# Performance work log

Hardware: AMD Instinct MI355X
Metric: run time of the kernel (lower is better)

The kernel has to match this reference:

```python
import jax, jax.numpy as jnp
import numpy as np

EPS = 1e-5
B, C, N = 2, 256, 65536


def conv1x1(x, W, b):
    # Conv1d with kernel_size=1: (B,Cin,N) x (Cout,Cin) -> (B,Cout,N)
    return jnp.einsum('oc,bcn->bon', W, x) + b[None, :, None]


def instance_norm(x):
    # InstanceNorm1d, affine=False, biased variance over the spatial dim
    m = jnp.mean(x, axis=-1, keepdims=True)
    v = jnp.var(x, axis=-1, keepdims=True)
    return (x - m) * jax.lax.rsqrt(v + EPS)


def mesh_conv(x, gemm, W, b):
    # MeshCNN MeshConv: gather self + 4 one-ring neighbor edges, symmetric fns, (1,5) conv.
    Bb, Cc, E = x.shape
    xp = jnp.concatenate([jnp.zeros((Bb, Cc, 1), x.dtype), x], axis=2)  # pad slot 0 (for -1/missing)
    eid = jnp.broadcast_to(jnp.arange(E, dtype=gemm.dtype)[None, :, None], (Bb, E, 1))
    Gi = jnp.concatenate([eid, gemm], axis=2) + 1                      # (B,E,5), +1 shift for pad row
    xt = xp.transpose(0, 2, 1)                                          # (B,E+1,C)
    f = jax.vmap(lambda xb, gb: xb[gb])(xt, Gi)                         # (B,E,5,C) gather
    f = f.transpose(0, 3, 1, 2)                                         # (B,C,E,5)
    f0, f1, f2, f3, f4 = (f[..., i] for i in range(5))
    g = jnp.stack([f0, f1 + f3, f2 + f4, jnp.abs(f1 - f3), jnp.abs(f2 - f4)], axis=-1)
    # Conv2d(Cin,Cout,(1,5)) over (B,C,E,5) -> (B,Cout,E)
    return jnp.einsum('ock,bcek->boe', W, g) + b[None, :, None]


def setup_inputs() -> dict:
    key = jax.random.key(0)
    ks = jax.random.split(key, 20)
    s = 0.05
    inp = {
        'x_0': jax.random.normal(ks[0], (B, C, N), jnp.float32),
        'x_1': jax.random.normal(ks[1], (B, C, N), jnp.float32),
        'gemm': jax.random.randint(ks[2], (B, N, 4), 0, N, jnp.int32),
        # conv_a / conv_b: C -> C//4
        'Wa': jax.random.normal(ks[3], (C // 4, C), jnp.float32) * s,
        'ba': jax.random.normal(ks[4], (C // 4,), jnp.float32) * s,
        'Wb': jax.random.normal(ks[5], (C // 4, C), jnp.float32) * s,
        'bb': jax.random.normal(ks[6], (C // 4,), jnp.float32) * s,
        # conv_a_local / conv_b_local: C//2 -> C//2
        'Wal': jax.random.normal(ks[7], (C // 2, C // 2), jnp.float32) * s,
        'bal': jax.random.normal(ks[8], (C // 2,), jnp.float32) * s,
        'Wbl': jax.random.normal(ks[9], (C // 2, C // 2), jnp.float32) * s,
        'bbl': jax.random.normal(ks[10], (C // 2,), jnp.float32) * s,
        # MeshConv weights: (Cout, Cin, 5)
        'Wat': jax.random.normal(ks[11], (C // 2, C // 2, 5), jnp.float32) * s,
        'bat': jax.random.normal(ks[12], (C // 2,), jnp.float32) * s,
        'Wbt': jax.random.normal(ks[13], (C // 2, C // 2, 5), jnp.float32) * s,
        'bbt': jax.random.normal(ks[14], (C // 2,), jnp.float32) * s,
        # fuse convs: C -> C
        'Waf': jax.random.normal(ks[15], (C, C), jnp.float32) * s,
        'baf': jax.random.normal(ks[16], (C,), jnp.float32) * s,
        'Wbf': jax.random.normal(ks[17], (C, C), jnp.float32) * s,
        'bbf': jax.random.normal(ks[18], (C,), jnp.float32) * s,
    }
    return inp


def reference(x_0, x_1, gemm, Wa, ba, Wb, bb, Wal, bal, Wbl, bbl,
              Wat, bat, Wbt, bbt, Waf, baf, Wbf, bbf):
    x_a = conv1x1(x_0, Wa, ba)
    x_b = conv1x1(x_1, Wb, bb)
    x_all = jnp.concatenate([x_a, x_b], axis=1)          # (B, C/2, N)
    a_local = conv1x1(x_all, Wal, bal)
    a_tri = mesh_conv(x_all, gemm, Wat, bat)
    x_a_two = jnp.concatenate([a_local, a_tri], axis=1)  # (B, C, N)
    b_local = conv1x1(x_all, Wbl, bbl)
    b_tri = mesh_conv(x_all, gemm, Wbt, bbt)
    x_b_two = jnp.concatenate([b_local, b_tri], axis=1)
    wa = jax.nn.sigmoid(instance_norm(conv1x1(x_a_two, Waf, baf)))
    wb = jax.nn.sigmoid(instance_norm(conv1x1(x_b_two, Wbf, bbf)))
    w = jax.nn.softmax(jnp.stack([wa, wb], axis=1), axis=1)  # (B,2,C,N)
    return x_0 * w[:, 0] + x_1 * w[:, 1]
```

## Files before the change

kernel.cpp:

```cpp
#include <hip/hip_runtime.h>
#include <stdint.h>

#define NEDGE 65536

typedef __attribute__((ext_vector_type(4))) float f32x4;
typedef __attribute__((ext_vector_type(8))) __bf16 bf16x8;

__device__ __forceinline__ uint16_t f2bf(float f) {
  union { float f; uint32_t u; } v; v.f = f;
  uint32_t r = v.u + 0x7FFFu + ((v.u >> 16) & 1u);
  return (uint16_t)(r >> 16);
}
__device__ __forceinline__ float bflo(uint32_t u) {
  union { uint32_t u; float f; } v; v.u = u << 16; return v.f;
}
__device__ __forceinline__ float bfhi(uint32_t u) {
  union { uint32_t u; float f; } v; v.u = u & 0xFFFF0000u; return v.f;
}
__device__ __forceinline__ uint32_t packbf(float lo, float hi) {
  return (uint32_t)f2bf(lo) | ((uint32_t)f2bf(hi) << 16);
}
__device__ __forceinline__ void gload_lds16(const void* g, void* l) {
  __builtin_amdgcn_global_load_lds(
      (__attribute__((address_space(1))) uint32_t*)(uintptr_t)g,
      (__attribute__((address_space(3))) uint32_t*)l, 16, 0, 0);
}
__device__ __forceinline__ float sigm(float z) { return 1.0f / (1.0f + __expf(-z)); }

__global__ void k_compose(const float* __restrict__ Wal, const float* __restrict__ Wbl,
                          const float* __restrict__ Wat, const float* __restrict__ Wbt,
                          const float* __restrict__ Waf, const float* __restrict__ Wbf,
                          uint16_t* __restrict__ Wt) {
  int id = blockIdx.x * 256 + threadIdx.x;
  if (id >= 512 * 640) return;
  int j = id / 640, kk = id % 640;
  const float* Wf = (j < 256) ? Waf : Wbf;
  const float* Wl = (j < 256) ? Wal : Wbl;
  const float* Wr = (j < 256) ? Wat : Wbt;
  int jj = j & 255;
  float acc = 0.f;
  if (kk < 128) {
    int c = kk;
    for (int o = 0; o < 128; ++o) acc += Wl[o * 128 + c] * Wf[jj * 256 + o];
    for (int o = 0; o < 128; ++o) acc += Wr[(o * 128 + c) * 5 + 0] * Wf[jj * 256 + 128 + o];
  } else {
    int blkid = (kk - 128) >> 7;
    int gk = (blkid == 0) ? 1 : (blkid == 1) ? 3 : (blkid == 2) ? 2 : 4;
    int c = (kk - 128) & 127;
    for (int o = 0; o < 128; ++o) acc += Wr[(o * 128 + c) * 5 + gk] * Wf[jj * 256 + 128 + o];
  }
  Wt[j * 640 + kk] = f2bf(acc);
}

__global__ void k_bias(const float* __restrict__ bal, const float* __restrict__ bat,
                       const float* __restrict__ baf, const float* __restrict__ bbl,
                       const float* __restrict__ bbt, const float* __restrict__ bbf,
                       const float* __restrict__ Waf, const float* __restrict__ Wbf,
                       float* __restrict__ biasF) {
  int id = blockIdx.x * 256 + threadIdx.x;
  if (id >= 512) return;
  const float* Wf = (id < 256) ? Waf : Wbf;
  const float* bl = (id < 256) ? bal : bbl;
  const float* bt = (id < 256) ? bat : bbt;
  const float* bsf = (id < 256) ? baf : bbf;
  int jj = id & 255;
  float acc = bsf[jj];
  for (int o = 0; o < 128; ++o) acc += Wf[jj * 256 + o] * bl[o];
  for (int o = 0; o < 128; ++o) acc += Wf[jj * 256 + 128 + o] * bt[o];
  biasF[id] = acc;
}

__global__ void k_wt1(const float* __restrict__ Wa, const float* __restrict__ Wb,
                      uint16_t* __restrict__ W1bf) {
  int id = blockIdx.x * 256 + threadIdx.x;
  if (id >= 2 * 64 * 256) return;
  int side = id >> 14, r = id & 16383;
  W1bf[id] = f2bf(side ? Wb[r] : Wa[r]);
}

__global__ __launch_bounds__(256) void k1_xa(
    const float* __restrict__ x0, const float* __restrict__ x1,
    const uint16_t* __restrict__ W1bf, const float* __restrict__ ba,
    const float* __restrict__ bb, uint16_t* __restrict__ XA) {
  __shared__ __align__(16) float Xs[3][32 * 128];
  __shared__ __align__(16) uint16_t Bs[64 * 256];
  int t = threadIdx.x;
  int side = blockIdx.y, b = blockIdx.z;
  int n0 = blockIdx.x * 128;
  const float* xin = (side ? x1 : x0) + (size_t)b * 256 * NEDGE + n0;
  const uint16_t* wsrc = W1bf + side * 64 * 256;

#pragma unroll
  for (int q = 0; q < 8; ++q) {
    int s = q * 256 + t;
    int j = s >> 5, pb = s & 31;
    int lb = pb ^ (j & 7);
    gload_lds16(wsrc + j * 256 + lb * 8, &Bs[s * 8]);
  }
#pragma unroll
  for (int c = 0; c < 2; ++c) {
#pragma unroll
    for (int q = 0; q < 4; ++q) {
      int s = q * 256 + t;
      int cl = s >> 5, pb = s & 31;
      int lb = pb ^ (((cl >> 3) & 3) << 2);
      gload_lds16(xin + (size_t)(c * 32 + cl) * NEDGE + lb * 4, &Xs[c][s * 4]);
    }
  }

  int wv = t >> 6, l = t & 63;
  int m = l & 15, g = l >> 4;

  f32x4 acc[2][4];
  f32x4 zero = {0.f, 0.f, 0.f, 0.f};
#pragma unroll
  for (int rf = 0; rf < 2; ++rf)
#pragma unroll
    for (int cf = 0; cf < 4; ++cf) acc[rf][cf] = zero;

#pragma unroll
  for (int ks = 0; ks < 8; ++ks) {
    if (ks < 6) {
      const float* xc = xin + (size_t)(ks + 2) * 32 * NEDGE;
#pragma unroll
      for (int q = 0; q < 4; ++q) {
        int s = q * 256 + t;
        int cl = s >> 5, pb = s & 31;
        int lb = pb ^ (((cl >> 3) & 3) << 2);
        gload_lds16(xc + (size_t)cl * NEDGE + lb * 4, &Xs[(ks + 2) % 3][s * 4]);
      }
      asm volatile("s_waitcnt vmcnt(8)" ::: "memory");
    } else if (ks == 6) {
      asm volatile("s_waitcnt vmcnt(4)" ::: "memory");
    } else {
      asm volatile("s_waitcnt vmcnt(0)" ::: "memory");
    }
    __builtin_amdgcn_sched_barrier(0);
    __builtin_amdgcn_s_barrier();

    const float* Xb = Xs[ks % 3];
    bf16x8 bfr[4];
#pragma unroll
    for (int cf = 0; cf < 4; ++cf) {
      int jloc = cf * 16 + m;
      int pbb = (ks * 4 + g) ^ (jloc & 7);
      bfr[cf] = *(const bf16x8*)&Bs[jloc * 256 + pbb * 8];
    }
#pragma unroll
    for (int rf = 0; rf < 2; ++rf) {
      int nloc = rf * 64 + wv * 16 + m;
      int phys = (nloc >> 2) ^ (g << 2);
      const float* base = Xb + phys * 4 + (nloc & 3);
      float xv[8];
#pragma unroll
      for (int i = 0; i < 8; ++i) xv[i] = base[(g * 8 + i) * 128];
      union { bf16x8 v; __bf16 e[8]; } af;
#pragma unroll
      for (int i = 0; i < 8; ++i) af.e[i] = (__bf16)xv[i];
#pragma unroll
      for (int cf = 0; cf < 4; ++cf)
        acc[rf][cf] = __builtin_amdgcn_mfma_f32_16x16x32_bf16(af.v, bfr[cf], acc[rf][cf], 0, 0, 0);
    }
    __builtin_amdgcn_s_barrier();
  }

  const float* bias = side ? bb : ba;
  uint16_t* XAb = XA + ((size_t)b * NEDGE + n0) * 128 + side * 64;
#pragma unroll
  for (int rf = 0; rf < 2; ++rf)
#pragma unroll
    for (int cf = 0; cf < 4; ++cf) {
      float bv = bias[cf * 16 + m];
#pragma unroll
      for (int q = 0; q < 4; ++q) {
        int row = rf * 64 + wv * 16 + g * 4 + q;
        XAb[(size_t)row * 128 + cf * 16 + m] = f2bf(acc[rf][cf][q] + bv);
      }
    }
}

__device__ __forceinline__ void feat_pair(uint32_t u1, uint32_t u3, uint32_t& s, uint32_t& d) {
  float a1 = bflo(u1), b1 = bfhi(u1), a3 = bflo(u3), b3 = bfhi(u3);
  s = packbf(a1 + a3, b1 + b3);
  d = packbf(fabsf(a1 - a3), fabsf(b1 - b3));
}
__global__ void k2_gather(const uint16_t* __restrict__ XAb, const int* __restrict__ gidx,
                          uint16_t* __restrict__ G) {
  int t = threadIdx.x;
  int wid = t >> 6, lane = t & 63;
  int wbase = (blockIdx.x * 4 + wid) * 16;
  int g = lane >> 4, sl = lane & 15;
  for (int it = 0; it < 4; ++it) {
    int e0 = wbase + it * 4;
    int myidx = 0;
    if (lane < 16) myidx = gidx[(size_t)e0 * 4 + lane];
    int e = e0 + g;
    int i1 = __shfl(myidx, g * 4 + 0);
    int i2 = __shfl(myidx, g * 4 + 1);
    int i3 = __shfl(myidx, g * 4 + 2);
    int i4 = __shfl(myidx, g * 4 + 3);
    uint4 v1 = ((const uint4*)(XAb + (size_t)i1 * 128))[sl];
    uint4 v2 = ((const uint4*)(XAb + (size_t)i2 * 128))[sl];
    uint4 v3 = ((const uint4*)(XAb + (size_t)i3 * 128))[sl];
    uint4 v4 = ((const uint4*)(XAb + (size_t)i4 * 128))[sl];
    uint4 F1, F3, F2, F4;
    feat_pair(v1.x, v3.x, F1.x, F3.x); feat_pair(v1.y, v3.y, F1.y, F3.y);
    feat_pair(v1.z, v3.z, F1.z, F3.z); feat_pair(v1.w, v3.w, F1.w, F3.w);
    feat_pair(v2.x, v4.x, F2.x, F4.x); feat_pair(v2.y, v4.y, F2.y, F4.y);
    feat_pair(v2.z, v4.z, F2.z, F4.z); feat_pair(v2.w, v4.w, F2.w, F4.w);
    uint4* outr = (uint4*)(G + (size_t)e * 512);
    outr[sl] = F1; outr[16 + sl] = F3; outr[32 + sl] = F2; outr[48 + sl] = F4;
  }
}

__global__ __launch_bounds__(256, 2) void k3_gemm(
    const uint16_t* __restrict__ XAb, const uint16_t* __restrict__ G,
    const uint16_t* __restrict__ Wt, const float* __restrict__ biasF,
    uint16_t* __restrict__ Y) {
  __shared__ __align__(16) uint16_t As[2][128 * 64];
  __shared__ __align__(16) uint16_t Bs2[2][128 * 64];
  int bx = blockIdx.y;
  int by = blockIdx.x;
  int t = threadIdx.x;
  int ebase = bx * 128;
  int jbase = by * 128;
  int wid = t >> 6, lane = t & 63;
  int wr = wid >> 1, wc = wid & 1;
  int m = lane & 15, half = lane >> 4;

  f32x4 acc[4][4];
  f32x4 zero = {0.f, 0.f, 0.f, 0.f};
#pragma unroll
  for (int r = 0; r < 4; ++r)
#pragma unroll
    for (int c = 0; c < 4; ++c) acc[r][c] = zero;

#define K3_STAGE(s_, bi)                                                        \
  do {                                                                          \
    const uint16_t* srcb; size_t rstr; int koff;                                \
    if ((s_) < 2) { srcb = XAb; rstr = 128; koff = (s_) * 64; }                 \
    else          { srcb = G;   rstr = 512; koff = ((s_) - 2) * 64; }           \
    _Pragma("unroll")                                                           \
    for (int i = 0; i < 4; ++i) {                                               \
      int slot = i * 256 + t; int r = slot >> 3, c16 = slot & 7;                \
      gload_lds16(srcb + (size_t)(ebase + r) * rstr + koff + (c16 ^ (r & 7)) * 8, \
                  &As[bi][slot * 8]);                                           \
    }                                                                           \
    _Pragma("unroll")                                                           \
    for (int i = 0; i < 4; ++i) {                                               \
      int slot = i * 256 + t; int r = slot >> 3, c16 = slot & 7;                \
      gload_lds16(Wt + (size_t)(jbase + r) * 640 + (s_) * 64 + (c16 ^ (r & 7)) * 8, \
                  &Bs2[bi][slot * 8]);                                          \
    }                                                                           \
  } while (0)

  K3_STAGE(0, 0);

#pragma unroll
  for (int s = 0; s < 10; ++s) {
    if (s < 9) {
      K3_STAGE(s + 1, (s + 1) & 1);
      asm volatile("s_waitcnt vmcnt(8)" ::: "memory");
    } else {
      asm volatile("s_waitcnt vmcnt(0)" ::: "memory");
    }
    __builtin_amdgcn_sched_barrier(0);
    __builtin_amdgcn_s_barrier();

    const uint16_t* Ab = As[s & 1];
    const uint16_t* Bb = Bs2[s & 1];
#pragma unroll
    for (int kit = 0; kit < 2; ++kit) {
      bf16x8 af[4], bf[4];
#pragma unroll
      for (int r = 0; r < 4; ++r) {
        int row = wr * 64 + r * 16 + m;
        af[r] = *(const bf16x8*)&Ab[row * 64 + ((kit * 4 + half) ^ (m & 7)) * 8];
      }
#pragma unroll
      for (int cf = 0; cf < 4; ++cf) {
        int row = wc * 64 + cf * 16 + m;
        bf[cf] = *(const bf16x8*)&Bb[row * 64 + ((kit * 4 + half) ^ (m & 7)) * 8];
      }
#pragma unroll
      for (int r = 0; r < 4; ++r)
#pragma unroll
        for (int cf = 0; cf < 4; ++cf)
          acc[r][cf] = __builtin_amdgcn_mfma_f32_16x16x32_bf16(af[r], bf[cf], acc[r][cf], 0, 0, 0);
    }
    __builtin_amdgcn_s_barrier();
  }
#undef K3_STAGE

#pragma unroll
  for (int cf = 0; cf < 4; ++cf) {
    int col = jbase + wc * 64 + cf * 16 + m;
    float bv = biasF[col];
#pragma unroll
    for (int r = 0; r < 4; ++r) {
      int rowb = ebase + wr * 64 + r * 16 + half * 4;
#pragma unroll
      for (int q = 0; q < 4; ++q) {
        float v = acc[r][cf][q] + bv;
        Y[(size_t)(rowb + q) * 512 + col] = f2bf(v);
      }
    }
  }
}

__global__ void k3b1(const uint16_t* __restrict__ Y, float* __restrict__ part) {
  int t = threadIdx.x, ch = blockIdx.x;
  const uint32_t* Y32 = (const uint32_t*)Y;
  float s1a = 0, s2a = 0, s1b = 0, s2b = 0;
  size_t base = (size_t)ch * 128 * 256 + t;
  for (int r = 0; r < 128; ++r) {
    uint32_t v = Y32[base + (size_t)r * 256];
    float x = bflo(v), y = bfhi(v);
    s1a += x; s2a += x * x; s1b += y; s2b += y * y;
  }
  float* p = part + ((size_t)ch * 512 + 2 * t) * 2;
  p[0] = s1a; p[1] = s2a; p[2] = s1b; p[3] = s2b;
}
__global__ void k3b2(const float* __restrict__ part, float* __restrict__ statF) {
  int col = blockIdx.x, t = threadIdx.x;
  float s1 = 0, s2 = 0;
  for (int k = t; k < 512; k += 128) {
    const float* p = part + ((size_t)k * 512 + col) * 2;
    s1 += p[0]; s2 += p[1];
  }
  for (int off = 32; off; off >>= 1) { s1 += __shfl_down(s1, off); s2 += __shfl_down(s2, off); }
  __shared__ float sh[4];
  if ((t & 63) == 0) { sh[(t >> 6) * 2] = s1; sh[(t >> 6) * 2 + 1] = s2; }
  __syncthreads();
  if (t == 0) {
    s1 = sh[0] + sh[2]; s2 = sh[1] + sh[3];
    float mean = s1 * (1.0f / 65536.0f);
    float var = s2 * (1.0f / 65536.0f) - mean * mean;
    statF[col * 2] = mean;
    statF[col * 2 + 1] = rsqrtf(var + 1e-5f);
  }
}

__global__ __launch_bounds__(256) void k4_final(
    const uint16_t* __restrict__ Y, const float* __restrict__ statF,
    const float* __restrict__ x0b, const float* __restrict__ x1b,
    float* __restrict__ outb) {
  __shared__ float W0[128][65];
  __shared__ float mA[128], rA[128], mB[128], rB[128];
  int t = threadIdx.x;
  int n0 = blockIdx.x * 64;
  int ch = blockIdx.y;
  if (t < 128) {
    mA[t] = statF[(ch * 128 + t) * 2];
    rA[t] = statF[(ch * 128 + t) * 2 + 1];
  } else {
    int q = t - 128;
    mB[q] = statF[(256 + ch * 128 + q) * 2];
    rB[q] = statF[(256 + ch * 128 + q) * 2 + 1];
  }
  __syncthreads();
  const char* Ybase = (const char*)Y;
  for (int i = t; i < 64 * 64; i += 256) {
    int row = i >> 6, cp = i & 63;
    const char* yr = Ybase + (size_t)(n0 + row) * 1024;
    uint32_t ya2 = *(const uint32_t*)(yr + ch * 256 + cp * 4);
    uint32_t yb2 = *(const uint32_t*)(yr + 512 + ch * 256 + cp * 4);
    int c0 = 2 * cp, c1 = 2 * cp + 1;
    float wa0 = sigm((bflo(ya2) - mA[c0]) * rA[c0]);
    float wa1 = sigm((bfhi(ya2) - mA[c1]) * rA[c1]);
    float wb0 = sigm((bflo(yb2) - mB[c0]) * rB[c0]);
    float wb1 = sigm((bfhi(yb2) - mB[c1]) * rB[c1]);
    W0[c0][row] = sigm(wa0 - wb0);
    W0[c1][row] = sigm(wa1 - wb1);
  }
  __syncthreads();
  int nn = t & 63, cg = t >> 6;
  for (int cc = cg; cc < 128; cc += 4) {
    int c = ch * 128 + cc;
    size_t gi = (size_t)c * NEDGE + n0 + nn;
    float w0 = W0[cc][nn];
    outb[gi] = x0b[gi] * w0 + x1b[gi] * (1.0f - w0);
  }
}

extern "C" void kernel_launch(void* const* d_in, const int* in_sizes, int n_in,
                              void* d_out, int out_size, void* d_ws, size_t ws_size,
                              hipStream_t stream) {
  const float* x0 = (const float*)d_in[0];
  const float* x1 = (const float*)d_in[1];
  const int* gemm = (const int*)d_in[2];
  const float* Wa = (const float*)d_in[3];
  const float* ba = (const float*)d_in[4];
  const float* Wb = (const float*)d_in[5];
  const float* bb = (const float*)d_in[6];
  const float* Wal = (const float*)d_in[7];
  const float* bal = (const float*)d_in[8];
  const float* Wbl = (const float*)d_in[9];
  const float* bbl = (const float*)d_in[10];
  const float* Wat = (const float*)d_in[11];
  const float* bat = (const float*)d_in[12];
  const float* Wbt = (const float*)d_in[13];
  const float* bbt = (const float*)d_in[14];
  const float* Waf = (const float*)d_in[15];
  const float* baf = (const float*)d_in[16];
  const float* Wbf = (const float*)d_in[17];
  const float* bbf = (const float*)d_in[18];
  float* out = (float*)d_out;

  char* ws = (char*)d_ws;
  uint16_t* XA   = (uint16_t*)ws;
  uint16_t* G    = (uint16_t*)(ws + 33554432);
  uint16_t* Yb   = (uint16_t*)(ws + 100663296);
  uint16_t* Wt   = (uint16_t*)(ws + 167772160);
  uint16_t* W1bf = (uint16_t*)(ws + 168427520);
  float*    biasF= (float*)(ws + 168558592);
  float*    part = (float*)(ws + 168560640);
  float*    statF= (float*)(ws + 170657792);

  k_compose<<<dim3(1280), dim3(256), 0, stream>>>(Wal, Wbl, Wat, Wbt, Waf, Wbf, Wt);
  k_bias<<<dim3(2), dim3(256), 0, stream>>>(bal, bat, baf, bbl, bbt, bbf, Waf, Wbf, biasF);
  k_wt1<<<dim3(128), dim3(256), 0, stream>>>(Wa, Wb, W1bf);
  k1_xa<<<dim3(512, 2, 2), dim3(256), 0, stream>>>(x0, x1, W1bf, ba, bb, XA);

  for (int b = 0; b < 2; ++b) {
    const uint16_t* XAb = XA + (size_t)b * NEDGE * 128;
    k2_gather<<<dim3(1024), dim3(256), 0, stream>>>(XAb, gemm + (size_t)b * NEDGE * 4, G);
    k3_gemm<<<dim3(4, 512), dim3(256), 0, stream>>>(XAb, G, Wt, biasF, Yb);
    k3b1<<<dim3(512), dim3(256), 0, stream>>>(Yb, part);
    k3b2<<<dim3(512), dim3(128), 0, stream>>>(part, statF + b * 1024);
    k4_final<<<dim3(1024, 2), dim3(256), 0, stream>>>(
        Yb, statF + b * 1024, x0 + (size_t)b * 256 * NEDGE,
        x1 + (size_t)b * 256 * NEDGE, out + (size_t)b * 256 * NEDGE);
  }
}
```

Baseline: 428.9 us.

## Restage k1 input through registers into transposed bf16 LDS with larger tile

The first projection kernel now loads x with register f32x4 loads, converts to bf16 and writes a transposed, swizzled layout in LDS. Each MFMA A fragment then comes from two 64-bit LDS reads instead of eight scalar fp32 reads plus conversion. The tile grows to 256 edges per block with register double-buffering replacing the triple-buffered async LDS copies, which halves the grid. The cost is more registers (a larger accumulator plus two register staging sets), which may lower occupancy, and the async-copy overlap is replaced by register prefetch.

```diff
diff --git a/kernel.cpp b/kernel.cpp
--- a/kernel.cpp
+++ b/kernel.cpp
@@ -82,11 +82,11 @@
     const float* __restrict__ x0, const float* __restrict__ x1,
     const uint16_t* __restrict__ W1bf, const float* __restrict__ ba,
     const float* __restrict__ bb, uint16_t* __restrict__ XA) {
-  __shared__ __align__(16) float Xs[3][32 * 128];
+  __shared__ __align__(16) uint64_t XT[2][256 * 9];
   __shared__ __align__(16) uint16_t Bs[64 * 256];
   int t = threadIdx.x;
   int side = blockIdx.y, b = blockIdx.z;
-  int n0 = blockIdx.x * 128;
+  int n0 = blockIdx.x * 256;
   const float* xin = (side ? x1 : x0) + (size_t)b * 256 * NEDGE + n0;
   const uint16_t* wsrc = W1bf + side * 64 * 256;
 
@@ -97,48 +97,58 @@
     int lb = pb ^ (j & 7);
     gload_lds16(wsrc + j * 256 + lb * 8, &Bs[s * 8]);
   }
-#pragma unroll
-  for (int c = 0; c < 2; ++c) {
-#pragma unroll
-    for (int q = 0; q < 4; ++q) {
-      int s = q * 256 + t;
-      int cl = s >> 5, pb = s & 31;
-      int lb = pb ^ (((cl >> 3) & 3) << 2);
-      gload_lds16(xin + (size_t)(c * 32 + cl) * NEDGE + lb * 4, &Xs[c][s * 4]);
-    }
-  }
+  asm volatile("s_waitcnt vmcnt(0)" ::: "memory");
+
+  const int c4a = t >> 6, n4 = t & 63;
+  const int keyw = (n4 >> 1) & 7;
+
+  f32x4 rA[8], rB[8];
+  auto load_set = [&](f32x4* r, int ks) {
+#pragma unroll
+    for (int sl = 0; sl < 2; ++sl) {
+      int c4 = c4a + sl * 4;
+      const float* base = xin + (size_t)(ks * 32 + c4 * 4) * NEDGE + n4 * 4;
+#pragma unroll
+      for (int i = 0; i < 4; ++i)
+        r[sl * 4 + i] = *(const f32x4*)(base + (size_t)i * NEDGE);
+    }
+  };
+  auto write_set = [&](int buf, f32x4* r) {
+#pragma unroll
+    for (int sl = 0; sl < 2; ++sl) {
+      int c4 = c4a + sl * 4;
+      int cp = c4 ^ keyw;
+#pragma unroll
+      for (int j = 0; j < 4; ++j) {
+        uint32_t lo = packbf(r[sl * 4 + 0][j], r[sl * 4 + 1][j]);
+        uint32_t hi = packbf(r[sl * 4 + 2][j], r[sl * 4 + 3][j]);
+        XT[buf][(size_t)(n4 * 4 + j) * 9 + cp] = (uint64_t)lo | ((uint64_t)hi << 32);
+      }
+    }
+  };
+
+  load_set(rA, 0);
+  load_set(rB, 1);
 
   int wv = t >> 6, l = t & 63;
   int m = l & 15, g = l >> 4;
 
-  f32x4 acc[2][4];
+  f32x4 acc[4][4];
   f32x4 zero = {0.f, 0.f, 0.f, 0.f};
 #pragma unroll
-  for (int rf = 0; rf < 2; ++rf)
+  for (int rf = 0; rf < 4; ++rf)
 #pragma unroll
     for (int cf = 0; cf < 4; ++cf) acc[rf][cf] = zero;
 
 #pragma unroll
   for (int ks = 0; ks < 8; ++ks) {
-    if (ks < 6) {
-      const float* xc = xin + (size_t)(ks + 2) * 32 * NEDGE;
-#pragma unroll
-      for (int q = 0; q < 4; ++q) {
-        int s = q * 256 + t;
-        int cl = s >> 5, pb = s & 31;
-        int lb = pb ^ (((cl >> 3) & 3) << 2);
-        gload_lds16(xc + (size_t)cl * NEDGE + lb * 4, &Xs[(ks + 2) % 3][s * 4]);
-      }
-      asm volatile("s_waitcnt vmcnt(8)" ::: "memory");
-    } else if (ks == 6) {
-      asm volatile("s_waitcnt vmcnt(4)" ::: "memory");
-    } else {
-      asm volatile("s_waitcnt vmcnt(0)" ::: "memory");
-    }
+    f32x4* cur = (ks & 1) ? rB : rA;
+    write_set(ks & 1, cur);
+    if (ks < 6) load_set(cur, ks + 2);
+    asm volatile("s_waitcnt lgkmcnt(0)" ::: "memory");
+    __builtin_amdgcn_s_barrier();
     __builtin_amdgcn_sched_barrier(0);
-    __builtin_amdgcn_s_barrier();
-
-    const float* Xb = Xs[ks % 3];
+
     bf16x8 bfr[4];
 #pragma unroll
     for (int cf = 0; cf < 4; ++cf) {
@@ -147,27 +157,22 @@
       bfr[cf] = *(const bf16x8*)&Bs[jloc * 256 + pbb * 8];
     }
 #pragma unroll
-    for (int rf = 0; rf < 2; ++rf) {
-      int nloc = rf * 64 + wv * 16 + m;
-      int phys = (nloc >> 2) ^ (g << 2);
-      const float* base = Xb + phys * 4 + (nloc & 3);
-      float xv[8];
-#pragma unroll
-      for (int i = 0; i < 8; ++i) xv[i] = base[(g * 8 + i) * 128];
-      union { bf16x8 v; __bf16 e[8]; } af;
-#pragma unroll
-      for (int i = 0; i < 8; ++i) af.e[i] = (__bf16)xv[i];
+    for (int rf = 0; rf < 4; ++rf) {
+      int n = rf * 64 + wv * 16 + m;
+      int key = (n >> 3) & 7;
+      union { uint64_t u[2]; bf16x8 v; } af;
+      af.u[0] = XT[ks & 1][(size_t)n * 9 + ((2 * g) ^ key)];
+      af.u[1] = XT[ks & 1][(size_t)n * 9 + ((2 * g + 1) ^ key)];
 #pragma unroll
       for (int cf = 0; cf < 4; ++cf)
         acc[rf][cf] = __builtin_amdgcn_mfma_f32_16x16x32_bf16(af.v, bfr[cf], acc[rf][cf], 0, 0, 0);
     }
-    __builtin_amdgcn_s_barrier();
   }
 
   const float* bias = side ? bb : ba;
   uint16_t* XAb = XA + ((size_t)b * NEDGE + n0) * 128 + side * 64;
 #pragma unroll
-  for (int rf = 0; rf < 2; ++rf)
+  for (int rf = 0; rf < 4; ++rf)
 #pragma unroll
     for (int cf = 0; cf < 4; ++cf) {
       float bv = bias[cf * 16 + m];
@@ -420,7 +425,7 @@
   k_compose<<<dim3(1280), dim3(256), 0, stream>>>(Wal, Wbl, Wat, Wbt, Waf, Wbf, Wt);
   k_bias<<<dim3(2), dim3(256), 0, stream>>>(bal, bat, baf, bbl, bbt, bbf, Waf, Wbf, biasF);
   k_wt1<<<dim3(128), dim3(256), 0, stream>>>(Wa, Wb, W1bf);
-  k1_xa<<<dim3(512, 2, 2), dim3(256), 0, stream>>>(x0, x1, W1bf, ba, bb, XA);
+  k1_xa<<<dim3(256, 2, 2), dim3(256), 0, stream>>>(x0, x1, W1bf, ba, bb, XA);
 
   for (int b = 0; b < 2; ++b) {
     const uint16_t* XAb = XA + (size_t)b * NEDGE * 128;
```

Result: no change. 425.8 us (-0.7%).

## Fuse neighbor gather and stats reduction into mesh GEMM; transpose MFMA operands

Applied to the files above, without the earlier changes.

The separate gather kernel, which wrote a 4x-wide feature buffer G, is removed. The GEMM now loads neighbor rows from XA into registers, builds the sum and abs-diff features, and writes them to LDS, pipelining this with the weight loads. The GEMM tile grows to 128x256 with 512 threads, and the epilogue computes the per-channel sum and sum-of-squares partials, so the k3b1 pass that re-read Y is dropped. The k1 and k3 MFMA operand order is swapped so each lane can store packed bf16 vectors. This cuts the G write and read round-trip and one Y read, at the cost of exposed gather latency and higher register and LDS pressure inside the GEMM.

```diff
diff --git a/kernel.cpp b/kernel.cpp
--- a/kernel.cpp
+++ b/kernel.cpp
@@ -5,6 +5,9 @@
 
 typedef __attribute__((ext_vector_type(4))) float f32x4;
 typedef __attribute__((ext_vector_type(8))) __bf16 bf16x8;
+
+#define VMCNT(n) asm volatile("s_waitcnt vmcnt(" #n ")" ::: "memory")
+#define VMCNT_LGKM0(n) asm volatile("s_waitcnt vmcnt(" #n ") lgkmcnt(0)" ::: "memory")
 
 __device__ __forceinline__ uint16_t f2bf(float f) {
   union { float f; uint32_t u; } v; v.f = f;
@@ -110,13 +113,19 @@
 
   int wv = t >> 6, l = t & 63;
   int m = l & 15, g = l >> 4;
+  int pcol[2];
+#pragma unroll
+  for (int nf = 0; nf < 2; ++nf) {
+    int n = wv * 32 + nf * 16 + m;
+    pcol[nf] = (((n >> 2) ^ (g << 2)) << 2) + (n & 3);
+  }
 
   f32x4 acc[2][4];
   f32x4 zero = {0.f, 0.f, 0.f, 0.f};
 #pragma unroll
-  for (int rf = 0; rf < 2; ++rf)
-#pragma unroll
-    for (int cf = 0; cf < 4; ++cf) acc[rf][cf] = zero;
+  for (int nf = 0; nf < 2; ++nf)
+#pragma unroll
+    for (int jf = 0; jf < 4; ++jf) acc[nf][jf] = zero;
 
 #pragma unroll
   for (int ks = 0; ks < 8; ++ks) {
@@ -129,104 +138,125 @@
         int lb = pb ^ (((cl >> 3) & 3) << 2);
         gload_lds16(xc + (size_t)cl * NEDGE + lb * 4, &Xs[(ks + 2) % 3][s * 4]);
       }
-      asm volatile("s_waitcnt vmcnt(8)" ::: "memory");
+      VMCNT(8);
     } else if (ks == 6) {
-      asm volatile("s_waitcnt vmcnt(4)" ::: "memory");
+      VMCNT(4);
     } else {
-      asm volatile("s_waitcnt vmcnt(0)" ::: "memory");
+      VMCNT(0);
     }
     __builtin_amdgcn_sched_barrier(0);
     __builtin_amdgcn_s_barrier();
 
     const float* Xb = Xs[ks % 3];
-    bf16x8 bfr[4];
-#pragma unroll
-    for (int cf = 0; cf < 4; ++cf) {
-      int jloc = cf * 16 + m;
+    bf16x8 af[4];
+#pragma unroll
+    for (int jf = 0; jf < 4; ++jf) {
+      int jloc = jf * 16 + m;
       int pbb = (ks * 4 + g) ^ (jloc & 7);
-      bfr[cf] = *(const bf16x8*)&Bs[jloc * 256 + pbb * 8];
-    }
-#pragma unroll
-    for (int rf = 0; rf < 2; ++rf) {
-      int nloc = rf * 64 + wv * 16 + m;
-      int phys = (nloc >> 2) ^ (g << 2);
-      const float* base = Xb + phys * 4 + (nloc & 3);
+      af[jf] = *(const bf16x8*)&Bs[jloc * 256 + pbb * 8];
+    }
+#pragma unroll
+    for (int nf = 0; nf < 2; ++nf) {
+      const float* base = Xb + g * 8 * 128 + pcol[nf];
       float xv[8];
 #pragma unroll
-      for (int i = 0; i < 8; ++i) xv[i] = base[(g * 8 + i) * 128];
-      union { bf16x8 v; __bf16 e[8]; } af;
-#pragma unroll
-      for (int i = 0; i < 8; ++i) af.e[i] = (__bf16)xv[i];
-#pragma unroll
-      for (int cf = 0; cf < 4; ++cf)
-        acc[rf][cf] = __builtin_amdgcn_mfma_f32_16x16x32_bf16(af.v, bfr[cf], acc[rf][cf], 0, 0, 0);
+      for (int i = 0; i < 8; ++i) xv[i] = base[i * 128];
+      union { bf16x8 v; uint32_t u[4]; } bx;
+      bx.u[0] = packbf(xv[0], xv[1]);
+      bx.u[1] = packbf(xv[2], xv[3]);
+      bx.u[2] = packbf(xv[4], xv[5]);
+      bx.u[3] = packbf(xv[6], xv[7]);
+#pragma unroll
+      for (int jf = 0; jf < 4; ++jf)
+        acc[nf][jf] = __builtin_amdgcn_mfma_f32_16x16x32_bf16(af[jf], bx.v, acc[nf][jf], 0, 0, 0);
     }
     __builtin_amdgcn_s_barrier();
   }
 
   const float* bias = side ? bb : ba;
-  uint16_t* XAb = XA + ((size_t)b * NEDGE + n0) * 128 + side * 64;
-#pragma unroll
-  for (int rf = 0; rf < 2; ++rf)
-#pragma unroll
-    for (int cf = 0; cf < 4; ++cf) {
-      float bv = bias[cf * 16 + m];
-#pragma unroll
-      for (int q = 0; q < 4; ++q) {
-        int row = rf * 64 + wv * 16 + g * 4 + q;
-        XAb[(size_t)row * 128 + cf * 16 + m] = f2bf(acc[rf][cf][q] + bv);
-      }
-    }
-}
-
-__device__ __forceinline__ void feat_pair(uint32_t u1, uint32_t u3, uint32_t& s, uint32_t& d) {
-  float a1 = bflo(u1), b1 = bfhi(u1), a3 = bflo(u3), b3 = bfhi(u3);
-  s = packbf(a1 + a3, b1 + b3);
-  d = packbf(fabsf(a1 - a3), fabsf(b1 - b3));
-}
-__global__ void k2_gather(const uint16_t* __restrict__ XAb, const int* __restrict__ gidx,
-                          uint16_t* __restrict__ G) {
+  uint16_t* XAb = XA + (size_t)b * NEDGE * 128;
+#pragma unroll
+  for (int jf = 0; jf < 4; ++jf) {
+    f32x4 bv = *(const f32x4*)(bias + jf * 16 + g * 4);
+#pragma unroll
+    for (int nf = 0; nf < 2; ++nf) {
+      int n = n0 + wv * 32 + nf * 16 + m;
+      uint2 o;
+      o.x = packbf(acc[nf][jf][0] + bv[0], acc[nf][jf][1] + bv[1]);
+      o.y = packbf(acc[nf][jf][2] + bv[2], acc[nf][jf][3] + bv[3]);
+      *(uint2*)(XAb + (size_t)n * 128 + side * 64 + jf * 16 + g * 4) = o;
+    }
+  }
+}
+
+__global__ __launch_bounds__(512) void k23_gemm(
+    const uint16_t* __restrict__ XAb, const int* __restrict__ gidx,
+    const uint16_t* __restrict__ Wt, const float* __restrict__ biasF,
+    uint16_t* __restrict__ Y, float* __restrict__ part) {
+  __shared__ __align__(16) uint16_t As[2][128 * 64];
+  __shared__ __align__(16) uint16_t Bs2[2][256 * 64];
+  __shared__ int gi[512];
+  __shared__ float sL[2][256][2];
   int t = threadIdx.x;
+  int jbase = blockIdx.x * 256;
+  int bx = blockIdx.y;
+  int ebase = bx * 128;
   int wid = t >> 6, lane = t & 63;
-  int wbase = (blockIdx.x * 4 + wid) * 16;
-  int g = lane >> 4, sl = lane & 15;
-  for (int it = 0; it < 4; ++it) {
-    int e0 = wbase + it * 4;
-    int myidx = 0;
-    if (lane < 16) myidx = gidx[(size_t)e0 * 4 + lane];
-    int e = e0 + g;
-    int i1 = __shfl(myidx, g * 4 + 0);
-    int i2 = __shfl(myidx, g * 4 + 1);
-    int i3 = __shfl(myidx, g * 4 + 2);
-    int i4 = __shfl(myidx, g * 4 + 3);
-    uint4 v1 = ((const uint4*)(XAb + (size_t)i1 * 128))[sl];
-    uint4 v2 = ((const uint4*)(XAb + (size_t)i2 * 128))[sl];
-    uint4 v3 = ((const uint4*)(XAb + (size_t)i3 * 128))[sl];
-    uint4 v4 = ((const uint4*)(XAb + (size_t)i4 * 128))[sl];
-    uint4 F1, F3, F2, F4;
-    feat_pair(v1.x, v3.x, F1.x, F3.x); feat_pair(v1.y, v3.y, F1.y, F3.y);
-    feat_pair(v1.z, v3.z, F1.z, F3.z); feat_pair(v1.w, v3.w, F1.w, F3.w);
-    feat_pair(v2.x, v4.x, F2.x, F4.x); feat_pair(v2.y, v4.y, F2.y, F4.y);
-    feat_pair(v2.z, v4.z, F2.z, F4.z); feat_pair(v2.w, v4.w, F2.w, F4.w);
-    uint4* outr = (uint4*)(G + (size_t)e * 512);
-    outr[sl] = F1; outr[16 + sl] = F3; outr[32 + sl] = F2; outr[48 + sl] = F4;
-  }
-}
-
-__global__ __launch_bounds__(256, 2) void k3_gemm(
-    const uint16_t* __restrict__ XAb, const uint16_t* __restrict__ G,
-    const uint16_t* __restrict__ Wt, const float* __restrict__ biasF,
-    uint16_t* __restrict__ Y) {
-  __shared__ __align__(16) uint16_t As[2][128 * 64];
-  __shared__ __align__(16) uint16_t Bs2[2][128 * 64];
-  int bx = blockIdx.y;
-  int by = blockIdx.x;
-  int t = threadIdx.x;
-  int ebase = bx * 128;
-  int jbase = by * 128;
-  int wid = t >> 6, lane = t & 63;
-  int wr = wid >> 1, wc = wid & 1;
-  int m = lane & 15, half = lane >> 4;
+  int wr = wid >> 2, wc = wid & 3;
+  int m = lane & 15, g = lane >> 4;
+
+  gi[t] = gidx[(size_t)ebase * 4 + t];
+  __syncthreads();
+
+  const int r0 = t >> 3, cc = t & 7;
+  int iP13[2], iQ13[2], iP24[2], iQ24[2];
+#pragma unroll
+  for (int q2 = 0; q2 < 2; ++q2) {
+    int r = r0 + q2 * 64;
+    iP13[q2] = gi[r * 4 + 0]; iQ13[q2] = gi[r * 4 + 2];
+    iP24[q2] = gi[r * 4 + 1]; iQ24[q2] = gi[r * 4 + 3];
+  }
+
+  uint4 grP[2][2], grQ[2][2];
+
+#define ISSUE_GATH(v)                                                           \
+  do {                                                                          \
+    const int coffv = ((v) & 1) * 64;                                           \
+    const int pr = ((v) - 2) >> 2;              \
+    _Pragma("unroll")                                                           \
+    for (int q2 = 0; q2 < 2; ++q2) {                                            \
+      int ip = pr ? iP24[q2] : iP13[q2];                                        \
+      int iq = pr ? iQ24[q2] : iQ13[q2];                                        \
+      grP[(v) & 1][q2] = *(const uint4*)(XAb + (size_t)ip * 128 + coffv + cc * 8); \
+      grQ[(v) & 1][q2] = *(const uint4*)(XAb + (size_t)iq * 128 + coffv + cc * 8); \
+    }                                                                           \
+  } while (0)
+
+#define ISSUE_BS(s_)                                                            \
+  do {                                                                          \
+    _Pragma("unroll")                                                           \
+    for (int q = 0; q < 4; ++q) {                                               \
+      int slot = q * 512 + t; int r = slot >> 3, c16 = slot & 7;                \
+      gload_lds16(Wt + (size_t)(jbase + r) * 640 + (s_) * 64 + (c16 ^ (r & 7)) * 8, \
+                  &Bs2[(s_) & 1][slot * 8]);                                    \
+    }                                                                           \
+  } while (0)
+
+#define ISSUE_AS_DIRECT(s_)                                                     \
+  do {                                                                          \
+    _Pragma("unroll")                                                           \
+    for (int q = 0; q < 2; ++q) {                                               \
+      int slot = q * 512 + t; int r = slot >> 3, c16 = slot & 7;                \
+      gload_lds16(XAb + (size_t)(ebase + r) * 128 + (s_) * 64 + (c16 ^ (r & 7)) * 8, \
+                  &As[(s_) & 1][slot * 8]);                                     \
+    }                                                                           \
+  } while (0)
+
+  ISSUE_GATH(2);
+  ISSUE_AS_DIRECT(0);
+  ISSUE_BS(0);
+  ISSUE_AS_DIRECT(1);
+  ISSUE_BS(1);
 
   f32x4 acc[4][4];
   f32x4 zero = {0.f, 0.f, 0.f, 0.f};
@@ -235,92 +265,123 @@
 #pragma unroll
     for (int c = 0; c < 4; ++c) acc[r][c] = zero;
 
-#define K3_STAGE(s_, bi)                                                        \
-  do {                                                                          \
-    const uint16_t* srcb; size_t rstr; int koff;                                \
-    if ((s_) < 2) { srcb = XAb; rstr = 128; koff = (s_) * 64; }                 \
-    else          { srcb = G;   rstr = 512; koff = ((s_) - 2) * 64; }           \
-    _Pragma("unroll")                                                           \
-    for (int i = 0; i < 4; ++i) {                                               \
-      int slot = i * 256 + t; int r = slot >> 3, c16 = slot & 7;                \
-      gload_lds16(srcb + (size_t)(ebase + r) * rstr + koff + (c16 ^ (r & 7)) * 8, \
-                  &As[bi][slot * 8]);                                           \
-    }                                                                           \
-    _Pragma("unroll")                                                           \
-    for (int i = 0; i < 4; ++i) {                                               \
-      int slot = i * 256 + t; int r = slot >> 3, c16 = slot & 7;                \
-      gload_lds16(Wt + (size_t)(jbase + r) * 640 + (s_) * 64 + (c16 ^ (r & 7)) * 8, \
-                  &Bs2[bi][slot * 8]);                                          \
-    }                                                                           \
-  } while (0)
-
-  K3_STAGE(0, 0);
-
-#pragma unroll
-  for (int s = 0; s < 10; ++s) {
-    if (s < 9) {
-      K3_STAGE(s + 1, (s + 1) & 1);
-      asm volatile("s_waitcnt vmcnt(8)" ::: "memory");
-    } else {
-      asm volatile("s_waitcnt vmcnt(0)" ::: "memory");
-    }
+#pragma unroll
+  for (int u = 0; u < 10; ++u) {
+    const int su = u + 1;
+    if (su >= 2 && su <= 9) {
+      if (u == 1) { VMCNT(6); } else { VMCNT(4); }
+      const int sum_op = (((su - 2) >> 1) & 1) == 0;
+      const int bi = su & 1;
+#pragma unroll
+      for (int q2 = 0; q2 < 2; ++q2) {
+        int r = r0 + q2 * 64;
+        uint4 P = grP[bi][q2], Q = grQ[bi][q2];
+        uint4 R;
+        if (sum_op) {
+          R.x = packbf(bflo(P.x) + bflo(Q.x), bfhi(P.x) + bfhi(Q.x));
+          R.y = packbf(bflo(P.y) + bflo(Q.y), bfhi(P.y) + bfhi(Q.y));
+          R.z = packbf(bflo(P.z) + bflo(Q.z), bfhi(P.z) + bfhi(Q.z));
+          R.w = packbf(bflo(P.w) + bflo(Q.w), bfhi(P.w) + bfhi(Q.w));
+        } else {
+          R.x = packbf(fabsf(bflo(P.x) - bflo(Q.x)), fabsf(bfhi(P.x) - bfhi(Q.x)));
+          R.y = packbf(fabsf(bflo(P.y) - bflo(Q.y)), fabsf(bfhi(P.y) - bfhi(Q.y)));
+          R.z = packbf(fabsf(bflo(P.z) - bflo(Q.z)), fabsf(bfhi(P.z) - bfhi(Q.z)));
+          R.w = packbf(fabsf(bflo(P.w) - bflo(Q.w)), fabsf(bfhi(P.w) - bfhi(Q.w)));
+        }
+        *(uint4*)&As[bi][(r * 8 + (cc ^ (r & 7))) * 8] = R;
+      }
+    }
+    if (u + 2 >= 3 && u + 2 <= 9) ISSUE_GATH(u + 2);
+    if (su >= 2 && su <= 9) ISSUE_BS(su);
+    if (u == 0) { VMCNT_LGKM0(6); }
+    else if (u <= 7) { VMCNT_LGKM0(8); }
+    else if (u == 8) { VMCNT_LGKM0(4); }
+    else { VMCNT_LGKM0(0); }
     __builtin_amdgcn_sched_barrier(0);
     __builtin_amdgcn_s_barrier();
 
-    const uint16_t* Ab = As[s & 1];
-    const uint16_t* Bb = Bs2[s & 1];
+    const uint16_t* Ab = As[u & 1];
+    const uint16_t* Bb = Bs2[u & 1];
 #pragma unroll
     for (int kit = 0; kit < 2; ++kit) {
       bf16x8 af[4], bf[4];
 #pragma unroll
       for (int r = 0; r < 4; ++r) {
         int row = wr * 64 + r * 16 + m;
-        af[r] = *(const bf16x8*)&Ab[row * 64 + ((kit * 4 + half) ^ (m & 7)) * 8];
+        af[r] = *(const bf16x8*)&Ab[row * 64 + ((kit * 4 + g) ^ (m & 7)) * 8];
       }
 #pragma unroll
       for (int cf = 0; cf < 4; ++cf) {
         int row = wc * 64 + cf * 16 + m;
-        bf[cf] = *(const bf16x8*)&Bb[row * 64 + ((kit * 4 + half) ^ (m & 7)) * 8];
+        bf[cf] = *(const bf16x8*)&Bb[row * 64 + ((kit * 4 + g) ^ (m & 7)) * 8];
       }
 #pragma unroll
       for (int r = 0; r < 4; ++r)
 #pragma unroll
         for (int cf = 0; cf < 4; ++cf)
-          acc[r][cf] = __builtin_amdgcn_mfma_f32_16x16x32_bf16(af[r], bf[cf], acc[r][cf], 0, 0, 0);
+          acc[r][cf] = __builtin_amdgcn_mfma_f32_16x16x32_bf16(bf[cf], af[r], acc[r][cf], 0, 0, 0);
     }
     __builtin_amdgcn_s_barrier();
   }
-#undef K3_STAGE
+#undef ISSUE_GATH
+#undef ISSUE_BS
+#undef ISSUE_AS_DIRECT
+
+  float s1[4][4], s2[4][4];
+#pragma unroll
+  for (int cf = 0; cf < 4; ++cf)
+#pragma unroll
+    for (int q = 0; q < 4; ++q) { s1[cf][q] = 0.f; s2[cf][q] = 0.f; }
 
 #pragma unroll
   for (int cf = 0; cf < 4; ++cf) {
-    int col = jbase + wc * 64 + cf * 16 + m;
-    float bv = biasF[col];
+    f32x4 bv = *(const f32x4*)(biasF + jbase + wc * 64 + cf * 16 + g * 4);
 #pragma unroll
     for (int r = 0; r < 4; ++r) {
-      int rowb = ebase + wr * 64 + r * 16 + half * 4;
+      int eg = ebase + wr * 64 + r * 16 + m;
+      float v0 = acc[r][cf][0] + bv[0];
+      float v1 = acc[r][cf][1] + bv[1];
+      float v2 = acc[r][cf][2] + bv[2];
+      float v3 = acc[r][cf][3] + bv[3];
+      s1[cf][0] += v0; s2[cf][0] += v0 * v0;
+      s1[cf][1] += v1; s2[cf][1] += v1 * v1;
+      s1[cf][2] += v2; s2[cf][2] += v2 * v2;
+      s1[cf][3] += v3; s2[cf][3] += v3 * v3;
+      uint2 o;
+      o.x = packbf(v0, v1);
+      o.y = packbf(v2, v3);
+      *(uint2*)(Y + (size_t)eg * 512 + jbase + wc * 64 + cf * 16 + g * 4) = o;
+    }
+  }
+#pragma unroll
+  for (int cf = 0; cf < 4; ++cf)
+#pragma unroll
+    for (int q = 0; q < 4; ++q) {
+#pragma unroll
+      for (int off = 1; off < 16; off <<= 1) {
+        s1[cf][q] += __shfl_xor(s1[cf][q], off);
+        s2[cf][q] += __shfl_xor(s2[cf][q], off);
+      }
+    }
+  if (m == 0) {
+#pragma unroll
+    for (int cf = 0; cf < 4; ++cf)
 #pragma unroll
       for (int q = 0; q < 4; ++q) {
-        float v = acc[r][cf][q] + bv;
-        Y[(size_t)(rowb + q) * 512 + col] = f2bf(v);
-      }
-    }
-  }
-}
-
-__global__ void k3b1(const uint16_t* __restrict__ Y, float* __restrict__ part) {
-  int t = threadIdx.x, ch = blockIdx.x;
-  const uint32_t* Y32 = (const uint32_t*)Y;
-  float s1a = 0, s2a = 0, s1b = 0, s2b = 0;
-  size_t base = (size_t)ch * 128 * 256 + t;
-  for (int r = 0; r < 128; ++r) {
-    uint32_t v = Y32[base + (size_t)r * 256];
-    float x = bflo(v), y = bfhi(v);
-    s1a += x; s2a += x * x; s1b += y; s2b += y * y;
-  }
-  float* p = part + ((size_t)ch * 512 + 2 * t) * 2;
-  p[0] = s1a; p[1] = s2a; p[2] = s1b; p[3] = s2b;
-}
+        int jl = wc * 64 + cf * 16 + g * 4 + q;
+        sL[wr][jl][0] = s1[cf][q];
+        sL[wr][jl][1] = s2[cf][q];
+      }
+  }
+  __syncthreads();
+  if (t < 256) {
+    float a1 = sL[0][t][0] + sL[1][t][0];
+    float a2 = sL[0][t][1] + sL[1][t][1];
+    float* p = part + ((size_t)bx * 512 + jbase + t) * 2;
+    p[0] = a1; p[1] = a2;
+  }
+}
+
 __global__ void k3b2(const float* __restrict__ part, float* __restrict__ statF) {
   int col = blockIdx.x, t = threadIdx.x;
   float s1 = 0, s2 = 0;
@@ -409,13 +470,12 @@
 
   char* ws = (char*)d_ws;
   uint16_t* XA   = (uint16_t*)ws;
-  uint16_t* G    = (uint16_t*)(ws + 33554432);
-  uint16_t* Yb   = (uint16_t*)(ws + 100663296);
-  uint16_t* Wt   = (uint16_t*)(ws + 167772160);
-  uint16_t* W1bf = (uint16_t*)(ws + 168427520);
-  float*    biasF= (float*)(ws + 168558592);
-  float*    part = (float*)(ws + 168560640);
-  float*    statF= (float*)(ws + 170657792);
+  uint16_t* Yb   = (uint16_t*)(ws + 33554432);
+  uint16_t* Wt   = (uint16_t*)(ws + 100663296);
+  uint16_t* W1bf = (uint16_t*)(ws + 101318656);
+  float*    biasF= (float*)(ws + 101384192);
+  float*    part = (float*)(ws + 101386240);
+  float*    statF= (float*)(ws + 103483392);
 
   k_compose<<<dim3(1280), dim3(256), 0, stream>>>(Wal, Wbl, Wat, Wbt, Waf, Wbf, Wt);
   k_bias<<<dim3(2), dim3(256), 0, stream>>>(bal, bat, baf, bbl, bbt, bbf, Waf, Wbf, biasF);
@@ -424,9 +484,8 @@
 
   for (int b = 0; b < 2; ++b) {
     const uint16_t* XAb = XA + (size_t)b * NEDGE * 128;
-    k2_gather<<<dim3(1024), dim3(256), 0, stream>>>(XAb, gemm + (size_t)b * NEDGE * 4, G);
-    k3_gemm<<<dim3(4, 512), dim3(256), 0, stream>>>(XAb, G, Wt, biasF, Yb);
-    k3b1<<<dim3(512), dim3(256), 0, stream>>>(Yb, part);
+    k23_gemm<<<dim3(2, 512), dim3(512), 0, stream>>>(
+        XAb, gemm + (size_t)b * NEDGE * 4, Wt, biasF, Yb, part);
     k3b2<<<dim3(512), dim3(128), 0, stream>>>(part, statF + b * 1024);
     k4_final<<<dim3(1024, 2), dim3(256), 0, stream>>>(
         Yb, statF + b * 1024, x0 + (size_t)b * 256 * NEDGE,
```

New measurement: 412.6 us. -3.8%, faster.
